# Optimization experiments

Measured on AMD Instinct MI355X. Metric: run time of the kernel, lower is better.

## Reference

```python
import jax, jax.numpy as jnp
import numpy as np

B, T, I, H, O = 32, 512, 512, 1024, 512


def setup_inputs() -> dict:
    key = jax.random.key(0)
    ks = jax.random.split(key, 8)
    inv_h = 1.0 / np.sqrt(H)
    inv_i = 1.0 / np.sqrt(I)
    return {
        "x": jax.random.normal(ks[0], (B, T, I), jnp.float32),
        "h0": jax.random.normal(ks[1], (1, B, H), jnp.float32),
        # nn.RNN params (PyTorch layout: W_ih [H, I], W_hh [H, H])
        "W_ih": jax.random.uniform(ks[2], (H, I), jnp.float32, -inv_h, inv_h),
        "W_hh": jax.random.uniform(ks[3], (H, H), jnp.float32, -inv_h, inv_h),
        "b_ih": jax.random.uniform(ks[4], (H,), jnp.float32, -inv_h, inv_h),
        "b_hh": jax.random.uniform(ks[5], (H,), jnp.float32, -inv_h, inv_h),
        # final Linear(hidden_dim, output_dim): W_out [O, H]
        "W_out": jax.random.uniform(ks[6], (O, H), jnp.float32, -inv_h, inv_h),
        "b_out": jax.random.uniform(ks[7], (O,), jnp.float32, -inv_h, inv_h),
    }


def reference(x, h0, W_ih, W_hh, b_ih, b_hh, W_out, b_out):
    # Precompute input contribution for all timesteps: [B, T, H]
    pre = jnp.einsum('bti,hi->bth', x, W_ih) + b_ih

    def step(h, p_t):
        # h_t = tanh(x_t W_ih^T + b_ih + h_{t-1} W_hh^T + b_hh)
        h_new = jnp.tanh(p_t + h @ W_hh.T + b_hh)
        return h_new, h_new

    _, zs = jax.lax.scan(step, h0[0], jnp.swapaxes(pre, 0, 1))  # zs: [T, B, H]
    z = jnp.swapaxes(zs, 0, 1)  # [B, T, H]
    out = jax.nn.softmax(z @ W_out.T + b_out, axis=2)  # [B, T, O]
    return out, z
```

## Files before the change

kernel.cpp:

```cpp
#include <hip/hip_runtime.h>
#include <math.h>

#define B_ 32
#define T_ 512
#define I_ 512
#define H_ 1024
#define O_ 512
#define MT (B_*T_)

__device__ unsigned g_cnt[256];

__global__ __launch_bounds__(256)
void gemm_nt_bias(float* __restrict__ C, const float* __restrict__ A,
                  const float* __restrict__ Bm, const float* __restrict__ bias,
                  int M, int N, int K, unsigned* __restrict__ cnt) {
  __shared__ float As[16][132];
  __shared__ float Bs[16][132];
  const int tid = threadIdx.x;
  if (cnt != nullptr && blockIdx.x == 0 && blockIdx.y == 0) cnt[tid] = 0u;
  const int bm = blockIdx.x * 128;
  const int bn = blockIdx.y * 128;
  const int lr = tid >> 2;
  const int lc = (tid & 3) * 4;
  const int tm = (tid >> 4) * 8;
  const int tn = (tid & 15) * 8;

  float acc[8][8];
#pragma unroll
  for (int i = 0; i < 8; ++i)
#pragma unroll
    for (int j = 0; j < 8; ++j) acc[i][j] = 0.f;

  for (int k0 = 0; k0 < K; k0 += 16) {
    float4 a0 = *(const float4*)(A  + (size_t)(bm + lr)      * K + k0 + lc);
    float4 a1 = *(const float4*)(A  + (size_t)(bm + lr + 64) * K + k0 + lc);
    float4 b0 = *(const float4*)(Bm + (size_t)(bn + lr)      * K + k0 + lc);
    float4 b1 = *(const float4*)(Bm + (size_t)(bn + lr + 64) * K + k0 + lc);
    __syncthreads();
    As[lc+0][lr]    = a0.x; As[lc+1][lr]    = a0.y; As[lc+2][lr]    = a0.z; As[lc+3][lr]    = a0.w;
    As[lc+0][lr+64] = a1.x; As[lc+1][lr+64] = a1.y; As[lc+2][lr+64] = a1.z; As[lc+3][lr+64] = a1.w;
    Bs[lc+0][lr]    = b0.x; Bs[lc+1][lr]    = b0.y; Bs[lc+2][lr]    = b0.z; Bs[lc+3][lr]    = b0.w;
    Bs[lc+0][lr+64] = b1.x; Bs[lc+1][lr+64] = b1.y; Bs[lc+2][lr+64] = b1.z; Bs[lc+3][lr+64] = b1.w;
    __syncthreads();
#pragma unroll
    for (int k = 0; k < 16; ++k) {
      float a[8], b[8];
      *(float4*)&a[0] = *(const float4*)&As[k][tm];
      *(float4*)&a[4] = *(const float4*)&As[k][tm + 4];
      *(float4*)&b[0] = *(const float4*)&Bs[k][tn];
      *(float4*)&b[4] = *(const float4*)&Bs[k][tn + 4];
#pragma unroll
      for (int i = 0; i < 8; ++i)
#pragma unroll
        for (int j = 0; j < 8; ++j) acc[i][j] += a[i] * b[j];
    }
  }

  float bv[8];
#pragma unroll
  for (int j = 0; j < 8; ++j) bv[j] = bias[bn + tn + j];
#pragma unroll
  for (int i = 0; i < 8; ++i) {
    float* crow = C + (size_t)(bm + tm + i) * N + bn + tn;
    float4 o0 = {acc[i][0]+bv[0], acc[i][1]+bv[1], acc[i][2]+bv[2], acc[i][3]+bv[3]};
    float4 o1 = {acc[i][4]+bv[4], acc[i][5]+bv[5], acc[i][6]+bv[6], acc[i][7]+bv[7]};
    *(float4*)(crow)     = o0;
    *(float4*)(crow + 4) = o1;
  }
}

__global__ __launch_bounds__(512, 2)
void rnn_fused(float* __restrict__ z, const float* __restrict__ h0,
               const float* __restrict__ Whh, const float* __restrict__ bhh,
               unsigned* __restrict__ cnt) {
  __shared__ float hs[4][1024];

  const int tid = threadIdx.x;
  const int bg  = blockIdx.x & 7;
  const int js  = blockIdx.x >> 3;
  const int j0  = js * 32;
  const int b0  = bg * 4;
  unsigned* mycnt = cnt + bg * 32;

  const int jg   = tid >> 6;
  const int ksl  = tid & 63;
  const int w    = ksl >> 2;
  const int jj   = w >> 2;
  const int bb   = w & 3;
  const int srow = tid >> 7;
  const int sc   = tid & 127;

  float4 wr[4][4];
#pragma unroll
  for (int kc = 0; kc < 4; ++kc)
#pragma unroll
    for (int j = 0; j < 4; ++j)
      wr[kc][j] = *(const float4*)(Whh + (size_t)(j0 + jg*4 + j) * H_ + ksl*4 + kc*256);

  const float breg = bhh[j0 + jg*4 + jj];

  for (int t = 0; t < T_; ++t) {
    if (t) {
      __syncthreads();
      if (tid == 0) {
        __hip_atomic_fetch_add(mycnt, 1u, __ATOMIC_RELAXED, __HIP_MEMORY_SCOPE_AGENT);
        const unsigned target = 32u * (unsigned)t;
        while (__hip_atomic_load(mycnt, __ATOMIC_RELAXED, __HIP_MEMORY_SCOPE_AGENT) < target)
          __builtin_amdgcn_s_sleep(1);
      }
      __syncthreads();
    }

    const float* zpre = z + ((size_t)(b0 + bb) * T_ + t) * H_ + j0 + jg*4 + jj;
    const float* hrow = (t == 0)
        ? (h0 + (size_t)(b0 + srow) * H_ + sc * 4)
        : (z + ((size_t)(b0 + srow) * T_ + (t - 1)) * H_ + sc * 4);
    float pre; float4 ha, hb;
    asm volatile(
      "global_load_dword %0, %3, off sc0 sc1\n\t"
      "global_load_dwordx4 %1, %4, off sc0 sc1\n\t"
      "global_load_dwordx4 %2, %4, off offset:2048 sc0 sc1\n\t"
      "s_waitcnt vmcnt(0)"
      : "=&v"(pre), "=&v"(ha), "=&v"(hb)
      : "v"(zpre), "v"(hrow)
      : "memory");
    *(float4*)&hs[srow][sc * 4]       = ha;
    *(float4*)&hs[srow][sc * 4 + 512] = hb;
    __syncthreads();

    float acc[16];
#pragma unroll
    for (int m = 0; m < 16; ++m) acc[m] = 0.f;
#pragma unroll
    for (int kc = 0; kc < 4; ++kc) {
      const int k = ksl * 4 + kc * 256;
      float4 h0v = *(const float4*)&hs[0][k];
      float4 h1v = *(const float4*)&hs[1][k];
      float4 h2v = *(const float4*)&hs[2][k];
      float4 h3v = *(const float4*)&hs[3][k];
#pragma unroll
      for (int j = 0; j < 4; ++j) {
        float4 wv = wr[kc][j];
        acc[j*4+0] += wv.x*h0v.x + wv.y*h0v.y + wv.z*h0v.z + wv.w*h0v.w;
        acc[j*4+1] += wv.x*h1v.x + wv.y*h1v.y + wv.z*h1v.z + wv.w*h1v.w;
        acc[j*4+2] += wv.x*h2v.x + wv.y*h2v.y + wv.z*h2v.z + wv.w*h2v.w;
        acc[j*4+3] += wv.x*h3v.x + wv.y*h3v.y + wv.z*h3v.z + wv.w*h3v.w;
      }
    }

    const bool b5 = (ksl & 32) != 0;
    float r8[8];
#pragma unroll
    for (int m = 0; m < 8; ++m) {
      float keep = b5 ? acc[m+8] : acc[m];
      float send = b5 ? acc[m]   : acc[m+8];
      r8[m] = keep + __shfl_xor(send, 32, 64);
    }
    const bool b4 = (ksl & 16) != 0;
    float r4[4];
#pragma unroll
    for (int m = 0; m < 4; ++m) {
      float keep = b4 ? r8[m+4] : r8[m];
      float send = b4 ? r8[m]   : r8[m+4];
      r4[m] = keep + __shfl_xor(send, 16, 64);
    }
    const bool b3 = (ksl & 8) != 0;
    float r2[2];
#pragma unroll
    for (int m = 0; m < 2; ++m) {
      float keep = b3 ? r4[m+2] : r4[m];
      float send = b3 ? r4[m]   : r4[m+2];
      r2[m] = keep + __shfl_xor(send, 8, 64);
    }
    const bool b2 = (ksl & 4) != 0;
    float r1 = (b2 ? r2[1] : r2[0]) + __shfl_xor(b2 ? r2[0] : r2[1], 4, 64);
    r1 += __shfl_xor(r1, 2, 64);
    r1 += __shfl_xor(r1, 1, 64);

    if ((ksl & 3) == 0) {
      float v = tanhf(r1 + pre + breg);
      asm volatile("global_store_dword %0, %1, off sc0 sc1"
                   :: "v"(zpre), "v"(v) : "memory");
    }
    asm volatile("s_waitcnt vmcnt(0)" ::: "memory");
  }
}

__global__ __launch_bounds__(256)
void softmax_rows(float* __restrict__ P) {
  const int row  = blockIdx.x * 4 + (threadIdx.x >> 6);
  const int lane = threadIdx.x & 63;
  float* p = P + (size_t)row * O_;
  float4 v0 = *(const float4*)(p + lane * 4);
  float4 v1 = *(const float4*)(p + 256 + lane * 4);

  float m = fmaxf(fmaxf(fmaxf(v0.x, v0.y), fmaxf(v0.z, v0.w)),
                  fmaxf(fmaxf(v1.x, v1.y), fmaxf(v1.z, v1.w)));
#pragma unroll
  for (int off = 32; off; off >>= 1) m = fmaxf(m, __shfl_xor(m, off, 64));

  v0.x = __expf(v0.x - m); v0.y = __expf(v0.y - m);
  v0.z = __expf(v0.z - m); v0.w = __expf(v0.w - m);
  v1.x = __expf(v1.x - m); v1.y = __expf(v1.y - m);
  v1.z = __expf(v1.z - m); v1.w = __expf(v1.w - m);

  float s = v0.x + v0.y + v0.z + v0.w + v1.x + v1.y + v1.z + v1.w;
#pragma unroll
  for (int off = 32; off; off >>= 1) s += __shfl_xor(s, off, 64);
  const float inv = 1.f / s;

  v0.x *= inv; v0.y *= inv; v0.z *= inv; v0.w *= inv;
  v1.x *= inv; v1.y *= inv; v1.z *= inv; v1.w *= inv;
  *(float4*)(p + lane * 4)       = v0;
  *(float4*)(p + 256 + lane * 4) = v1;
}

extern "C" void kernel_launch(void* const* d_in, const int* in_sizes, int n_in,
                              void* d_out, int out_size, void* d_ws, size_t ws_size,
                              hipStream_t stream) {
  const float* x    = (const float*)d_in[0];
  const float* h0   = (const float*)d_in[1];
  const float* Wih  = (const float*)d_in[2];
  const float* Whh  = (const float*)d_in[3];
  const float* bih  = (const float*)d_in[4];
  const float* bhh  = (const float*)d_in[5];
  const float* Wout = (const float*)d_in[6];
  const float* bout = (const float*)d_in[7];

  float* outp = (float*)d_out;
  float* z    = (float*)d_out + (size_t)MT * O_;

  static unsigned* cnt = nullptr;
  if (cnt == nullptr) {
    void* p = nullptr;
    hipGetSymbolAddress(&p, HIP_SYMBOL(g_cnt));
    cnt = (unsigned*)p;
  }

  gemm_nt_bias<<<dim3(MT / 128, H_ / 128), 256, 0, stream>>>(z, x, Wih, bih, MT, H_, I_, cnt);

  {
    float* z_a = z; const float* h0_a = h0; const float* Whh_a = Whh;
    const float* bhh_a = bhh; unsigned* cnt_a = cnt;
    void* kargs[] = {&z_a, &h0_a, &Whh_a, &bhh_a, &cnt_a};
    hipLaunchCooperativeKernel((const void*)rnn_fused, dim3(256), dim3(512),
                               kargs, 0, stream);
  }

  gemm_nt_bias<<<dim3(MT / 128, O_ / 128), 256, 0, stream>>>(outp, z, Wout, bout, MT, O_, H_, nullptr);
  softmax_rows<<<dim3(MT / 4), 256, 0, stream>>>(outp);
}
```

Measured before the change: 2.123 ms.

## Replace atomic counter barrier with per-block flag array polled by every wave

Replaces the per-group atomic counter barrier, where one thread increments, spins and then releases the block through a second __syncthreads, with a flag array. Each block stores its timestep into its own flag slot, and every wave polls all 32 flags of its batch group in parallel using cross-lane __all, which drops the extra block barrier and the serialized atomic. The precomputed input load is also issued before the spin so its latency overlaps the wait. The risk is more polling traffic, and ordering now depends on sc0 sc1 store and load visibility rather than atomics.

```diff
diff --git a/kernel.cpp b/kernel.cpp
--- a/kernel.cpp
+++ b/kernel.cpp
@@ -17,7 +17,10 @@
   __shared__ float As[16][132];
   __shared__ float Bs[16][132];
   const int tid = threadIdx.x;
-  if (cnt != nullptr && blockIdx.x == 0 && blockIdx.y == 0) cnt[tid] = 0u;
+  if (cnt != nullptr && blockIdx.x == 0 && blockIdx.y == 0) {
+    asm volatile("global_store_dword %0, %1, off sc0 sc1"
+                 :: "v"(cnt + tid), "v"(0u) : "memory");
+  }
   const int bm = blockIdx.x * 128;
   const int bn = blockIdx.y * 128;
   const int lr = tid >> 2;
@@ -80,7 +83,7 @@
   const int js  = blockIdx.x >> 3;
   const int j0  = js * 32;
   const int b0  = bg * 4;
-  unsigned* mycnt = cnt + bg * 32;
+  unsigned* gflags = cnt + bg * 32;
 
   const int jg   = tid >> 6;
   const int ksl  = tid & 63;
@@ -89,6 +92,8 @@
   const int bb   = w & 3;
   const int srow = tid >> 7;
   const int sc   = tid & 127;
+  const int pl   = tid & 31;
+  const bool own = (pl == js);
 
   float4 wr[4][4];
 #pragma unroll
@@ -100,29 +105,37 @@
   const float breg = bhh[j0 + jg*4 + jj];
 
   for (int t = 0; t < T_; ++t) {
+    const float* zpre = z + ((size_t)(b0 + bb) * T_ + t) * H_ + j0 + jg*4 + jj;
+    float pre;
+
     if (t) {
       __syncthreads();
-      if (tid == 0) {
-        __hip_atomic_fetch_add(mycnt, 1u, __ATOMIC_RELAXED, __HIP_MEMORY_SCOPE_AGENT);
-        const unsigned target = 32u * (unsigned)t;
-        while (__hip_atomic_load(mycnt, __ATOMIC_RELAXED, __HIP_MEMORY_SCOPE_AGENT) < target)
-          __builtin_amdgcn_s_sleep(1);
-      }
-      __syncthreads();
-    }
-
-    const float* zpre = z + ((size_t)(b0 + bb) * T_ + t) * H_ + j0 + jg*4 + jj;
+      if (tid == 0)
+        asm volatile("global_store_dword %0, %1, off sc0 sc1"
+                     :: "v"(gflags + js), "v"((unsigned)t) : "memory");
+      asm volatile("global_load_dword %0, %1, off"
+                   : "=v"(pre) : "v"(zpre) : "memory");
+      unsigned fv;
+      do {
+        asm volatile("global_load_dword %0, %1, off sc0 sc1\n\t"
+                     "s_waitcnt vmcnt(0)"
+                     : "=v"(fv) : "v"(gflags + pl) : "memory");
+      } while (!__all(own || fv >= (unsigned)t));
+    } else {
+      asm volatile("global_load_dword %0, %1, off"
+                   : "=v"(pre) : "v"(zpre) : "memory");
+    }
+
     const float* hrow = (t == 0)
         ? (h0 + (size_t)(b0 + srow) * H_ + sc * 4)
         : (z + ((size_t)(b0 + srow) * T_ + (t - 1)) * H_ + sc * 4);
-    float pre; float4 ha, hb;
+    float4 ha, hb;
     asm volatile(
-      "global_load_dword %0, %3, off sc0 sc1\n\t"
-      "global_load_dwordx4 %1, %4, off sc0 sc1\n\t"
-      "global_load_dwordx4 %2, %4, off offset:2048 sc0 sc1\n\t"
+      "global_load_dwordx4 %0, %2, off sc0 sc1\n\t"
+      "global_load_dwordx4 %1, %2, off offset:2048 sc0 sc1\n\t"
       "s_waitcnt vmcnt(0)"
-      : "=&v"(pre), "=&v"(ha), "=&v"(hb)
-      : "v"(zpre), "v"(hrow)
+      : "=&v"(ha), "=&v"(hb)
+      : "v"(hrow)
       : "memory");
     *(float4*)&hs[srow][sc * 4]       = ha;
     *(float4*)&hs[srow][sc * 4 + 512] = hb;
```

New measurement: 2.257 ms. +6.3%, slower.

## Replace counter barrier with tagged double-buffered hidden-state exchange in RNN

Applied to the files above, without the earlier changes.

Drops the per-step atomic counter barrier and spin-wait in the recurrent kernel. Each hidden value is now published to a double-buffered global exchange buffer paired with its step tag. Consumers poll until every tag they need matches, so a block can proceed as soon as its inputs are ready instead of waiting for all peers. The preactivation load is issued early to overlap with the poll. In exchange, every exchanged value carries a tag, which doubles exchange traffic, and correctness depends on the zero-initialisation done in the GEMM and on tag ordering across the two buffers.

```diff
diff --git a/kernel.cpp b/kernel.cpp
--- a/kernel.cpp
+++ b/kernel.cpp
@@ -8,16 +8,24 @@
 #define O_ 512
 #define MT (B_*T_)
 
-__device__ unsigned g_cnt[256];
+__device__ float2 g_x[2 * B_ * H_];
 
 __global__ __launch_bounds__(256)
 void gemm_nt_bias(float* __restrict__ C, const float* __restrict__ A,
                   const float* __restrict__ Bm, const float* __restrict__ bias,
-                  int M, int N, int K, unsigned* __restrict__ cnt) {
+                  int M, int N, int K, float2* __restrict__ xbuf) {
   __shared__ float As[16][132];
   __shared__ float Bs[16][132];
   const int tid = threadIdx.x;
-  if (cnt != nullptr && blockIdx.x == 0 && blockIdx.y == 0) cnt[tid] = 0u;
+  if (xbuf != nullptr && blockIdx.y == 0) {
+    const int r = blockIdx.x * 256 + tid;
+    unsigned zero = 0u;
+    float* t0 = (float*)(xbuf + r) + 1;
+    float* t1 = (float*)(xbuf + r + 32768) + 1;
+    asm volatile("global_store_dword %0, %2, off sc0 sc1\n\t"
+                 "global_store_dword %1, %2, off sc0 sc1"
+                 :: "v"(t0), "v"(t1), "v"(zero) : "memory");
+  }
   const int bm = blockIdx.x * 128;
   const int bn = blockIdx.y * 128;
   const int lr = tid >> 2;
@@ -72,7 +80,7 @@
 __global__ __launch_bounds__(512, 2)
 void rnn_fused(float* __restrict__ z, const float* __restrict__ h0,
                const float* __restrict__ Whh, const float* __restrict__ bhh,
-               unsigned* __restrict__ cnt) {
+               float2* __restrict__ xbuf) {
   __shared__ float hs[4][1024];
 
   const int tid = threadIdx.x;
@@ -80,7 +88,6 @@
   const int js  = blockIdx.x >> 3;
   const int j0  = js * 32;
   const int b0  = bg * 4;
-  unsigned* mycnt = cnt + bg * 32;
 
   const int jg   = tid >> 6;
   const int ksl  = tid & 63;
@@ -100,32 +107,43 @@
   const float breg = bhh[j0 + jg*4 + jj];
 
   for (int t = 0; t < T_; ++t) {
-    if (t) {
-      __syncthreads();
-      if (tid == 0) {
-        __hip_atomic_fetch_add(mycnt, 1u, __ATOMIC_RELAXED, __HIP_MEMORY_SCOPE_AGENT);
-        const unsigned target = 32u * (unsigned)t;
-        while (__hip_atomic_load(mycnt, __ATOMIC_RELAXED, __HIP_MEMORY_SCOPE_AGENT) < target)
-          __builtin_amdgcn_s_sleep(1);
-      }
-      __syncthreads();
-    }
-
-    const float* zpre = z + ((size_t)(b0 + bb) * T_ + t) * H_ + j0 + jg*4 + jj;
-    const float* hrow = (t == 0)
-        ? (h0 + (size_t)(b0 + srow) * H_ + sc * 4)
-        : (z + ((size_t)(b0 + srow) * T_ + (t - 1)) * H_ + sc * 4);
-    float pre; float4 ha, hb;
-    asm volatile(
-      "global_load_dword %0, %3, off sc0 sc1\n\t"
-      "global_load_dwordx4 %1, %4, off sc0 sc1\n\t"
-      "global_load_dwordx4 %2, %4, off offset:2048 sc0 sc1\n\t"
-      "s_waitcnt vmcnt(0)"
-      : "=&v"(pre), "=&v"(ha), "=&v"(hb)
-      : "v"(zpre), "v"(hrow)
-      : "memory");
-    *(float4*)&hs[srow][sc * 4]       = ha;
-    *(float4*)&hs[srow][sc * 4 + 512] = hb;
+    float* zs = z + ((size_t)(b0 + bb) * T_ + t) * H_ + j0 + jg*4 + jj;
+    float pre;
+    asm volatile("global_load_dword %0, %1, off"
+                 : "=v"(pre) : "v"(zs) : "memory");
+
+    if (t == 0) {
+      const float* hrow = h0 + (size_t)(b0 + srow) * H_ + sc * 4;
+      float4 ha = *(const float4*)(hrow);
+      float4 hb = *(const float4*)(hrow + 512);
+      *(float4*)&hs[srow][sc * 4]       = ha;
+      *(float4*)&hs[srow][sc * 4 + 512] = hb;
+    } else {
+      const float2* xr  = xbuf + (size_t)((t - 1) & 1) * (B_ * H_)
+                               + (size_t)(b0 + srow) * H_ + sc * 4;
+      const float2* xr2 = xr + 512;
+      const unsigned tagt = (unsigned)t;
+      float4 p0, p1, p2, p3;
+      bool ok;
+      do {
+        asm volatile(
+          "global_load_dwordx4 %0, %4, off sc0 sc1\n\t"
+          "global_load_dwordx4 %1, %4, off offset:16 sc0 sc1\n\t"
+          "global_load_dwordx4 %2, %5, off sc0 sc1\n\t"
+          "global_load_dwordx4 %3, %5, off offset:16 sc0 sc1\n\t"
+          "s_waitcnt vmcnt(0)"
+          : "=&v"(p0), "=&v"(p1), "=&v"(p2), "=&v"(p3)
+          : "v"(xr), "v"(xr2) : "memory");
+        ok = __float_as_uint(p0.y) == tagt && __float_as_uint(p0.w) == tagt
+          && __float_as_uint(p1.y) == tagt && __float_as_uint(p1.w) == tagt
+          && __float_as_uint(p2.y) == tagt && __float_as_uint(p2.w) == tagt
+          && __float_as_uint(p3.y) == tagt && __float_as_uint(p3.w) == tagt;
+      } while (!__all(ok));
+      float4 ha = {p0.x, p0.z, p1.x, p1.z};
+      float4 hb = {p2.x, p2.z, p3.x, p3.z};
+      *(float4*)&hs[srow][sc * 4]       = ha;
+      *(float4*)&hs[srow][sc * 4 + 512] = hb;
+    }
     __syncthreads();
 
     float acc[16];
@@ -177,12 +195,19 @@
     r1 += __shfl_xor(r1, 2, 64);
     r1 += __shfl_xor(r1, 1, 64);
 
+    asm volatile("s_waitcnt vmcnt(0)" ::: "memory");
     if ((ksl & 3) == 0) {
       float v = tanhf(r1 + pre + breg);
-      asm volatile("global_store_dword %0, %1, off sc0 sc1"
-                   :: "v"(zpre), "v"(v) : "memory");
-    }
-    asm volatile("s_waitcnt vmcnt(0)" ::: "memory");
+      *zs = v;
+      if (t + 1 < T_) {
+        float2 pv; pv.x = v; pv.y = __uint_as_float((unsigned)(t + 1));
+        float2* xw = xbuf + (size_t)(t & 1) * (B_ * H_)
+                          + (size_t)(b0 + bb) * H_ + (j0 + jg*4 + jj);
+        asm volatile("global_store_dwordx2 %0, %1, off sc0 sc1"
+                     :: "v"(xw), "v"(pv) : "memory");
+      }
+    }
+    __syncthreads();
   }
 }
 
@@ -230,19 +255,19 @@
   float* outp = (float*)d_out;
   float* z    = (float*)d_out + (size_t)MT * O_;
 
-  static unsigned* cnt = nullptr;
-  if (cnt == nullptr) {
+  static float2* xbuf = nullptr;
+  if (xbuf == nullptr) {
     void* p = nullptr;
-    hipGetSymbolAddress(&p, HIP_SYMBOL(g_cnt));
-    cnt = (unsigned*)p;
-  }
-
-  gemm_nt_bias<<<dim3(MT / 128, H_ / 128), 256, 0, stream>>>(z, x, Wih, bih, MT, H_, I_, cnt);
+    hipGetSymbolAddress(&p, HIP_SYMBOL(g_x));
+    xbuf = (float2*)p;
+  }
+
+  gemm_nt_bias<<<dim3(MT / 128, H_ / 128), 256, 0, stream>>>(z, x, Wih, bih, MT, H_, I_, xbuf);
 
   {
     float* z_a = z; const float* h0_a = h0; const float* Whh_a = Whh;
-    const float* bhh_a = bhh; unsigned* cnt_a = cnt;
-    void* kargs[] = {&z_a, &h0_a, &Whh_a, &bhh_a, &cnt_a};
+    const float* bhh_a = bhh; float2* xbuf_a = xbuf;
+    void* kargs[] = {&z_a, &h0_a, &Whh_a, &bhh_a, &xbuf_a};
     hipLaunchCooperativeKernel((const void*)rnn_fused, dim3(256), dim3(512),
                                kargs, 0, stream);
   }
```

Result: slower. 2.330 ms (+9.8%).
